# Kernel tuning notes

Hardware: AMD Instinct MI355X
Metric: run time of the kernel (lower is better)

The kernel has to match this reference:

```python
import jax, jax.numpy as jnp
import numpy as np

NUM_VOXELS = 2_000_000
NUM_CLUSTS = 2000
NUM_EDGES = 16_000
IN_FEATS = 4      # columns 1:5 of data: x, y, z, value
HIDDEN = 128
LATENT = 64       # encoder output feature size


def setup_inputs() -> dict:
    key = jax.random.key(0)
    k1, k2, k3, k4, k5, k6, k7 = jax.random.split(key, 7)
    data = jax.random.normal(k1, (NUM_VOXELS, 5), dtype=jnp.float32)
    clust_ids = jax.random.randint(k2, (NUM_VOXELS,), 0, NUM_CLUSTS)
    edge_index = jax.random.randint(k3, (2, NUM_EDGES), 0, NUM_CLUSTS)
    # encoder (pool + MLP) parameters
    W1 = jax.random.normal(k4, (IN_FEATS, HIDDEN), dtype=jnp.float32) / np.sqrt(IN_FEATS)
    b1 = jnp.zeros((HIDDEN,), dtype=jnp.float32)
    W2 = jax.random.normal(k5, (HIDDEN, LATENT), dtype=jnp.float32) / np.sqrt(HIDDEN)
    b2 = jnp.zeros((LATENT,), dtype=jnp.float32)
    return {"data": data, "clust_ids": clust_ids, "edge_index": edge_index,
            "W1": W1, "b1": b1, "W2": W2, "b2": b2}


def reference(data, clust_ids, edge_index, W1, b1, W2, b2):
    # Vectorized replacement of the per-edge python loop:
    # the loop builds, per edge i, the union of voxels of clusters (e0, e1)
    # with batch column overwritten by i; the encoder then globally pools
    # per edge-id. Equivalent: per-cluster sums via one segment_sum pass,
    # then per-edge mean over the union of the two clusters.
    feat = data[:, 1:5]                                   # [N, 4]
    clust_sum = jax.ops.segment_sum(feat, clust_ids, num_segments=NUM_CLUSTS)  # [C, 4]
    clust_cnt = jax.ops.segment_sum(jnp.ones((data.shape[0],), dtype=feat.dtype),
                                    clust_ids, num_segments=NUM_CLUSTS)        # [C]
    e0, e1 = edge_index[0], edge_index[1]
    pooled = (clust_sum[e0] + clust_sum[e1]) / jnp.maximum(clust_cnt[e0] + clust_cnt[e1], 1.0)[:, None]  # [E, 4]
    h = jax.nn.relu(pooled @ W1 + b1)                     # [E, HIDDEN]
    feats = h @ W2 + b2                                   # [E, LATENT]
    return feats
```

## Files before the change

### kernel.cpp

```cpp
#include <hip/hip_runtime.h>

#define NUM_VOXELS 2000000
#define NUM_CLUSTS 2000
#define NUM_EDGES  16000

#define ST   2048
#define ACCN (5 * ST)

#define FSCALE 131072.0f
#define FINV   (1.0f / 131072.0f)

#define A_THREADS 1024
#define A_BLOCKS  512
#define NSLICE (ACCN / 256)
#define RED_CH 64

__device__ __forceinline__ int fxp(float v) {
    return __float2int_rn(v * FSCALE);
}

__global__ __launch_bounds__(A_THREADS) void seg_accum(
        const float* __restrict__ data,
        const int* __restrict__ cids,
        int* __restrict__ part) {
    __shared__ int ls[ACCN];
    for (int o = threadIdx.x; o < ACCN; o += A_THREADS) ls[o] = 0;
    __syncthreads();

    const int ngroups = NUM_VOXELS / 4;
    for (int g = blockIdx.x * A_THREADS + threadIdx.x; g < ngroups;
         g += gridDim.x * A_THREADS) {
        const float4* dp = (const float4*)(data + 20ull * (unsigned)g);
        float4 q0 = dp[0];
        float4 q1 = dp[1];
        float4 q2 = dp[2];
        float4 q3 = dp[3];
        float4 q4 = dp[4];
        int4 c4 = *(const int4*)(cids + 4ull * (unsigned)g);

        atomicAdd(&ls[0 * ST + c4.x], fxp(q0.y));
        atomicAdd(&ls[1 * ST + c4.x], fxp(q0.z));
        atomicAdd(&ls[2 * ST + c4.x], fxp(q0.w));
        atomicAdd(&ls[3 * ST + c4.x], fxp(q1.x));
        atomicAdd(&ls[4 * ST + c4.x], 1);
        atomicAdd(&ls[0 * ST + c4.y], fxp(q1.z));
        atomicAdd(&ls[1 * ST + c4.y], fxp(q1.w));
        atomicAdd(&ls[2 * ST + c4.y], fxp(q2.x));
        atomicAdd(&ls[3 * ST + c4.y], fxp(q2.y));
        atomicAdd(&ls[4 * ST + c4.y], 1);
        atomicAdd(&ls[0 * ST + c4.z], fxp(q2.w));
        atomicAdd(&ls[1 * ST + c4.z], fxp(q3.x));
        atomicAdd(&ls[2 * ST + c4.z], fxp(q3.y));
        atomicAdd(&ls[3 * ST + c4.z], fxp(q3.z));
        atomicAdd(&ls[4 * ST + c4.z], 1);
        atomicAdd(&ls[0 * ST + c4.w], fxp(q4.x));
        atomicAdd(&ls[1 * ST + c4.w], fxp(q4.y));
        atomicAdd(&ls[2 * ST + c4.w], fxp(q4.z));
        atomicAdd(&ls[3 * ST + c4.w], fxp(q4.w));
        atomicAdd(&ls[4 * ST + c4.w], 1);
    }
    __syncthreads();

    int* p = part + (size_t)blockIdx.x * ACCN;
    for (int o = threadIdx.x; o < ACCN; o += A_THREADS) p[o] = ls[o];
}

__global__ __launch_bounds__(A_THREADS) void seg_accum_atomic(
        const float* __restrict__ data,
        const int* __restrict__ cids,
        int* __restrict__ acc) {
    __shared__ int ls[ACCN];
    for (int o = threadIdx.x; o < ACCN; o += A_THREADS) ls[o] = 0;
    __syncthreads();
    const int ngroups = NUM_VOXELS / 4;
    for (int g = blockIdx.x * A_THREADS + threadIdx.x; g < ngroups;
         g += gridDim.x * A_THREADS) {
        const float4* dp = (const float4*)(data + 20ull * (unsigned)g);
        float4 q0 = dp[0], q1 = dp[1], q2 = dp[2], q3 = dp[3], q4 = dp[4];
        int4 c4 = *(const int4*)(cids + 4ull * (unsigned)g);
        atomicAdd(&ls[0 * ST + c4.x], fxp(q0.y));
        atomicAdd(&ls[1 * ST + c4.x], fxp(q0.z));
        atomicAdd(&ls[2 * ST + c4.x], fxp(q0.w));
        atomicAdd(&ls[3 * ST + c4.x], fxp(q1.x));
        atomicAdd(&ls[4 * ST + c4.x], 1);
        atomicAdd(&ls[0 * ST + c4.y], fxp(q1.z));
        atomicAdd(&ls[1 * ST + c4.y], fxp(q1.w));
        atomicAdd(&ls[2 * ST + c4.y], fxp(q2.x));
        atomicAdd(&ls[3 * ST + c4.y], fxp(q2.y));
        atomicAdd(&ls[4 * ST + c4.y], 1);
        atomicAdd(&ls[0 * ST + c4.z], fxp(q2.w));
        atomicAdd(&ls[1 * ST + c4.z], fxp(q3.x));
        atomicAdd(&ls[2 * ST + c4.z], fxp(q3.y));
        atomicAdd(&ls[3 * ST + c4.z], fxp(q3.z));
        atomicAdd(&ls[4 * ST + c4.z], 1);
        atomicAdd(&ls[0 * ST + c4.w], fxp(q4.x));
        atomicAdd(&ls[1 * ST + c4.w], fxp(q4.y));
        atomicAdd(&ls[2 * ST + c4.w], fxp(q4.z));
        atomicAdd(&ls[3 * ST + c4.w], fxp(q4.w));
        atomicAdd(&ls[4 * ST + c4.w], 1);
    }
    __syncthreads();
    for (int o = threadIdx.x; o < ACCN; o += A_THREADS) {
        int v = ls[o];
        if (v != 0) atomicAdd(&acc[o], v);
    }
}

__global__ __launch_bounds__(256) void seg_reduce(
        const int* __restrict__ part, int* __restrict__ acc) {
    const int i = blockIdx.x * 256 + threadIdx.x;
    const int* p = part + (size_t)blockIdx.y * RED_CH * ACCN + i;
    int s0 = 0, s1 = 0, s2 = 0, s3 = 0;
#pragma unroll
    for (int b = 0; b < RED_CH; b += 4) {
        s0 += p[(size_t)(b + 0) * ACCN];
        s1 += p[(size_t)(b + 1) * ACCN];
        s2 += p[(size_t)(b + 2) * ACCN];
        s3 += p[(size_t)(b + 3) * ACCN];
    }
    atomicAdd(&acc[i], (s0 + s1) + (s2 + s3));
}

#define E_BLOCKS 256
#define E_THREADS 256
#define E_WAVES (E_BLOCKS * (E_THREADS / 64))

__global__ __launch_bounds__(E_THREADS) void edge_mlp(
        const int* __restrict__ acc,
        const int* __restrict__ eidx,
        const float* __restrict__ W1, const float* __restrict__ b1,
        const float* __restrict__ W2, const float* __restrict__ b2,
        float* __restrict__ out) {
    __shared__ float sacc[ACCN];
    __shared__ float hbuf[E_THREADS / 64][128];
    const int lane = threadIdx.x & 63;
    const int w = threadIdx.x >> 6;
    const int wg = blockIdx.x * (E_THREADS / 64) + w;

    float w1a[4], w1b[4];
#pragma unroll
    for (int c = 0; c < 4; ++c) {
        w1a[c] = W1[c * 128 + lane];
        w1b[c] = W1[c * 128 + 64 + lane];
    }
    const float b1a = b1[lane];
    const float b1b = b1[64 + lane];
    const float b2j = b2[lane];
    float w2c[128];
#pragma unroll
    for (int k = 0; k < 128; ++k) w2c[k] = W2[k * 64 + lane];

    for (int o = threadIdx.x; o < ACCN; o += E_THREADS) {
        int v = acc[o];
        sacc[o] = (o < 4 * ST) ? (float)v * FINV : (float)v;
    }
    __syncthreads();

    for (int e = wg; e < NUM_EDGES; e += E_WAVES) {
        const int e0 = eidx[e];
        const int e1 = eidx[NUM_EDGES + e];
        const float cnt = sacc[4 * ST + e0] + sacc[4 * ST + e1];
        const float rden = 1.0f / fmaxf(cnt, 1.0f);
        const float p0 = (sacc[0 * ST + e0] + sacc[0 * ST + e1]) * rden;
        const float p1 = (sacc[1 * ST + e0] + sacc[1 * ST + e1]) * rden;
        const float p2 = (sacc[2 * ST + e0] + sacc[2 * ST + e1]) * rden;
        const float p3 = (sacc[3 * ST + e0] + sacc[3 * ST + e1]) * rden;

        float ha = b1a + p0 * w1a[0] + p1 * w1a[1] + p2 * w1a[2] + p3 * w1a[3];
        float hb = b1b + p0 * w1b[0] + p1 * w1b[1] + p2 * w1b[2] + p3 * w1b[3];
        ha = fmaxf(ha, 0.0f);
        hb = fmaxf(hb, 0.0f);

        hbuf[w][lane] = ha;
        hbuf[w][64 + lane] = hb;

        float o0 = b2j;
#pragma unroll
        for (int k = 0; k < 128; k += 4) {
            float4 h4 = *(const float4*)&hbuf[w][k];
            o0 += h4.x * w2c[k] + h4.y * w2c[k + 1] + h4.z * w2c[k + 2] +
                  h4.w * w2c[k + 3];
        }
        out[(size_t)e * 64 + lane] = o0;
    }
}

extern "C" void kernel_launch(void* const* d_in, const int* in_sizes, int n_in,
                              void* d_out, int out_size, void* d_ws, size_t ws_size,
                              hipStream_t stream) {
    const float* data = (const float*)d_in[0];
    const int* cids   = (const int*)d_in[1];
    const int* eidx   = (const int*)d_in[2];
    const float* W1   = (const float*)d_in[3];
    const float* b1   = (const float*)d_in[4];
    const float* W2   = (const float*)d_in[5];
    const float* b2   = (const float*)d_in[6];
    float* out = (float*)d_out;
    int* ws = (int*)d_ws;

    if (ws_size >= (size_t)(A_BLOCKS + 1) * ACCN * sizeof(int)) {
        int* part = ws;
        int* acc = ws + (size_t)A_BLOCKS * ACCN;
        hipMemsetAsync(acc, 0, ACCN * sizeof(int), stream);
        seg_accum<<<A_BLOCKS, A_THREADS, 0, stream>>>(data, cids, part);
        seg_reduce<<<dim3(NSLICE, A_BLOCKS / RED_CH), 256, 0, stream>>>(part, acc);
        edge_mlp<<<E_BLOCKS, E_THREADS, 0, stream>>>(acc, eidx, W1, b1, W2, b2, out);
    } else {
        int* acc = ws;
        hipMemsetAsync(acc, 0, ACCN * sizeof(int), stream);
        seg_accum_atomic<<<A_BLOCKS, A_THREADS, 0, stream>>>(data, cids, acc);
        edge_mlp<<<E_BLOCKS, E_THREADS, 0, stream>>>(acc, eidx, W1, b1, W2, b2, out);
    }
}
```

Baseline: 127.7 us.

## Pack two biased fixed-point sums per 64-bit LDS atomic and drop memset

The voxel accumulation packs two features into one 64-bit shared-memory atomic. Each feature is biased to a positive fixed-point value at a lower scale so the two halves cannot carry into each other, which cuts LDS atomics per voxel from five to three. The final atomic reduce and the memset are replaced by writing per-chunk partials that edge_mlp sums itself. Block count is halved, data loads use nontemporal hints, edge indices are prefetched, and the W2 dot product is split into four accumulators. In exchange, precision drops and correctness relies on per-cluster biased sums fitting in 32 bits.

```diff
diff --git a/kernel.cpp b/kernel.cpp
--- a/kernel.cpp
+++ b/kernel.cpp
@@ -7,57 +7,60 @@
 #define ST   2048
 #define ACCN (5 * ST)
 
-#define FSCALE 131072.0f
-#define FINV   (1.0f / 131072.0f)
-
+#define FSCALE  65536.0f
+#define FINV    (1.0f / 65536.0f)
+#define BIASF   8.0f
+#define BIAS_FS (8.0f * 65536.0f)
+
+#define A_BLOCKS  256
 #define A_THREADS 1024
-#define A_BLOCKS  512
-#define NSLICE (ACCN / 256)
-#define RED_CH 64
-
-__device__ __forceinline__ int fxp(float v) {
-    return __float2int_rn(v * FSCALE);
+#define RED_CH    64
+#define NCH       (A_BLOCKS / RED_CH)
+
+typedef float  f4v __attribute__((ext_vector_type(4)));
+typedef int    i4v __attribute__((ext_vector_type(4)));
+typedef unsigned long long u64;
+
+__device__ __forceinline__ u64 pack2(float a, float b) {
+    unsigned lo = (unsigned)__float2int_rn(fmaf(a, FSCALE, BIAS_FS));
+    unsigned hi = (unsigned)__float2int_rn(fmaf(b, FSCALE, BIAS_FS));
+    return (u64)lo | ((u64)hi << 32);
 }
 
 __global__ __launch_bounds__(A_THREADS) void seg_accum(
         const float* __restrict__ data,
         const int* __restrict__ cids,
         int* __restrict__ part) {
-    __shared__ int ls[ACCN];
+    __shared__ __align__(16) int ls[ACCN];
+    u64* s01 = (u64*)ls;
+    u64* s23 = (u64*)(ls + 4096);
+    int* scnt = ls + 8192;
     for (int o = threadIdx.x; o < ACCN; o += A_THREADS) ls[o] = 0;
     __syncthreads();
 
     const int ngroups = NUM_VOXELS / 4;
     for (int g = blockIdx.x * A_THREADS + threadIdx.x; g < ngroups;
          g += gridDim.x * A_THREADS) {
-        const float4* dp = (const float4*)(data + 20ull * (unsigned)g);
-        float4 q0 = dp[0];
-        float4 q1 = dp[1];
-        float4 q2 = dp[2];
-        float4 q3 = dp[3];
-        float4 q4 = dp[4];
-        int4 c4 = *(const int4*)(cids + 4ull * (unsigned)g);
-
-        atomicAdd(&ls[0 * ST + c4.x], fxp(q0.y));
-        atomicAdd(&ls[1 * ST + c4.x], fxp(q0.z));
-        atomicAdd(&ls[2 * ST + c4.x], fxp(q0.w));
-        atomicAdd(&ls[3 * ST + c4.x], fxp(q1.x));
-        atomicAdd(&ls[4 * ST + c4.x], 1);
-        atomicAdd(&ls[0 * ST + c4.y], fxp(q1.z));
-        atomicAdd(&ls[1 * ST + c4.y], fxp(q1.w));
-        atomicAdd(&ls[2 * ST + c4.y], fxp(q2.x));
-        atomicAdd(&ls[3 * ST + c4.y], fxp(q2.y));
-        atomicAdd(&ls[4 * ST + c4.y], 1);
-        atomicAdd(&ls[0 * ST + c4.z], fxp(q2.w));
-        atomicAdd(&ls[1 * ST + c4.z], fxp(q3.x));
-        atomicAdd(&ls[2 * ST + c4.z], fxp(q3.y));
-        atomicAdd(&ls[3 * ST + c4.z], fxp(q3.z));
-        atomicAdd(&ls[4 * ST + c4.z], 1);
-        atomicAdd(&ls[0 * ST + c4.w], fxp(q4.x));
-        atomicAdd(&ls[1 * ST + c4.w], fxp(q4.y));
-        atomicAdd(&ls[2 * ST + c4.w], fxp(q4.z));
-        atomicAdd(&ls[3 * ST + c4.w], fxp(q4.w));
-        atomicAdd(&ls[4 * ST + c4.w], 1);
+        const f4v* dp = (const f4v*)(data + 20ull * (unsigned)g);
+        f4v q0 = __builtin_nontemporal_load(dp + 0);
+        f4v q1 = __builtin_nontemporal_load(dp + 1);
+        f4v q2 = __builtin_nontemporal_load(dp + 2);
+        f4v q3 = __builtin_nontemporal_load(dp + 3);
+        f4v q4 = __builtin_nontemporal_load(dp + 4);
+        i4v c4 = __builtin_nontemporal_load((const i4v*)(cids + 4ull * (unsigned)g));
+
+        atomicAdd(&s01[c4.x], pack2(q0.y, q0.z));
+        atomicAdd(&s23[c4.x], pack2(q0.w, q1.x));
+        atomicAdd(&scnt[c4.x], 1);
+        atomicAdd(&s01[c4.y], pack2(q1.z, q1.w));
+        atomicAdd(&s23[c4.y], pack2(q2.x, q2.y));
+        atomicAdd(&scnt[c4.y], 1);
+        atomicAdd(&s01[c4.z], pack2(q2.w, q3.x));
+        atomicAdd(&s23[c4.z], pack2(q3.y, q3.z));
+        atomicAdd(&scnt[c4.z], 1);
+        atomicAdd(&s01[c4.w], pack2(q4.x, q4.y));
+        atomicAdd(&s23[c4.w], pack2(q4.z, q4.w));
+        atomicAdd(&scnt[c4.w], 1);
     }
     __syncthreads();
 
@@ -69,35 +72,30 @@
         const float* __restrict__ data,
         const int* __restrict__ cids,
         int* __restrict__ acc) {
-    __shared__ int ls[ACCN];
+    __shared__ __align__(16) int ls[ACCN];
+    u64* s01 = (u64*)ls;
+    u64* s23 = (u64*)(ls + 4096);
+    int* scnt = ls + 8192;
     for (int o = threadIdx.x; o < ACCN; o += A_THREADS) ls[o] = 0;
     __syncthreads();
     const int ngroups = NUM_VOXELS / 4;
     for (int g = blockIdx.x * A_THREADS + threadIdx.x; g < ngroups;
          g += gridDim.x * A_THREADS) {
-        const float4* dp = (const float4*)(data + 20ull * (unsigned)g);
-        float4 q0 = dp[0], q1 = dp[1], q2 = dp[2], q3 = dp[3], q4 = dp[4];
-        int4 c4 = *(const int4*)(cids + 4ull * (unsigned)g);
-        atomicAdd(&ls[0 * ST + c4.x], fxp(q0.y));
-        atomicAdd(&ls[1 * ST + c4.x], fxp(q0.z));
-        atomicAdd(&ls[2 * ST + c4.x], fxp(q0.w));
-        atomicAdd(&ls[3 * ST + c4.x], fxp(q1.x));
-        atomicAdd(&ls[4 * ST + c4.x], 1);
-        atomicAdd(&ls[0 * ST + c4.y], fxp(q1.z));
-        atomicAdd(&ls[1 * ST + c4.y], fxp(q1.w));
-        atomicAdd(&ls[2 * ST + c4.y], fxp(q2.x));
-        atomicAdd(&ls[3 * ST + c4.y], fxp(q2.y));
-        atomicAdd(&ls[4 * ST + c4.y], 1);
-        atomicAdd(&ls[0 * ST + c4.z], fxp(q2.w));
-        atomicAdd(&ls[1 * ST + c4.z], fxp(q3.x));
-        atomicAdd(&ls[2 * ST + c4.z], fxp(q3.y));
-        atomicAdd(&ls[3 * ST + c4.z], fxp(q3.z));
-        atomicAdd(&ls[4 * ST + c4.z], 1);
-        atomicAdd(&ls[0 * ST + c4.w], fxp(q4.x));
-        atomicAdd(&ls[1 * ST + c4.w], fxp(q4.y));
-        atomicAdd(&ls[2 * ST + c4.w], fxp(q4.z));
-        atomicAdd(&ls[3 * ST + c4.w], fxp(q4.w));
-        atomicAdd(&ls[4 * ST + c4.w], 1);
+        const f4v* dp = (const f4v*)(data + 20ull * (unsigned)g);
+        f4v q0 = dp[0], q1 = dp[1], q2 = dp[2], q3 = dp[3], q4 = dp[4];
+        i4v c4 = *(const i4v*)(cids + 4ull * (unsigned)g);
+        atomicAdd(&s01[c4.x], pack2(q0.y, q0.z));
+        atomicAdd(&s23[c4.x], pack2(q0.w, q1.x));
+        atomicAdd(&scnt[c4.x], 1);
+        atomicAdd(&s01[c4.y], pack2(q1.z, q1.w));
+        atomicAdd(&s23[c4.y], pack2(q2.x, q2.y));
+        atomicAdd(&scnt[c4.y], 1);
+        atomicAdd(&s01[c4.z], pack2(q2.w, q3.x));
+        atomicAdd(&s23[c4.z], pack2(q3.y, q3.z));
+        atomicAdd(&scnt[c4.z], 1);
+        atomicAdd(&s01[c4.w], pack2(q4.x, q4.y));
+        atomicAdd(&s23[c4.w], pack2(q4.z, q4.w));
+        atomicAdd(&scnt[c4.w], 1);
     }
     __syncthreads();
     for (int o = threadIdx.x; o < ACCN; o += A_THREADS) {
@@ -107,7 +105,7 @@
 }
 
 __global__ __launch_bounds__(256) void seg_reduce(
-        const int* __restrict__ part, int* __restrict__ acc) {
+        const int* __restrict__ part, int* __restrict__ part2) {
     const int i = blockIdx.x * 256 + threadIdx.x;
     const int* p = part + (size_t)blockIdx.y * RED_CH * ACCN + i;
     int s0 = 0, s1 = 0, s2 = 0, s3 = 0;
@@ -118,7 +116,7 @@
         s2 += p[(size_t)(b + 2) * ACCN];
         s3 += p[(size_t)(b + 3) * ACCN];
     }
-    atomicAdd(&acc[i], (s0 + s1) + (s2 + s3));
+    part2[(size_t)blockIdx.y * ACCN + i] = (s0 + s1) + (s2 + s3);
 }
 
 #define E_BLOCKS 256
@@ -126,7 +124,7 @@
 #define E_WAVES (E_BLOCKS * (E_THREADS / 64))
 
 __global__ __launch_bounds__(E_THREADS) void edge_mlp(
-        const int* __restrict__ acc,
+        const int* __restrict__ part2,
         const int* __restrict__ eidx,
         const float* __restrict__ W1, const float* __restrict__ b1,
         const float* __restrict__ W2, const float* __restrict__ b2,
@@ -151,20 +149,35 @@
     for (int k = 0; k < 128; ++k) w2c[k] = W2[k * 64 + lane];
 
     for (int o = threadIdx.x; o < ACCN; o += E_THREADS) {
-        int v = acc[o];
-        sacc[o] = (o < 4 * ST) ? (float)v * FINV : (float)v;
-    }
-    __syncthreads();
-
+        int s = part2[o] + part2[ACCN + o] + part2[2 * ACCN + o] +
+                part2[3 * ACCN + o];
+        sacc[o] = (o < 8192) ? (float)s * FINV : (float)s;
+    }
+    __syncthreads();
+
+    int e0 = 0, e1 = 0;
+    if (wg < NUM_EDGES) {
+        e0 = eidx[wg];
+        e1 = eidx[NUM_EDGES + wg];
+    }
     for (int e = wg; e < NUM_EDGES; e += E_WAVES) {
-        const int e0 = eidx[e];
-        const int e1 = eidx[NUM_EDGES + e];
-        const float cnt = sacc[4 * ST + e0] + sacc[4 * ST + e1];
+        const int ne = e + E_WAVES;
+        int n0 = 0, n1 = 0;
+        if (ne < NUM_EDGES) {
+            n0 = eidx[ne];
+            n1 = eidx[NUM_EDGES + ne];
+        }
+        const float cnt = sacc[8192 + e0] + sacc[8192 + e1];
         const float rden = 1.0f / fmaxf(cnt, 1.0f);
-        const float p0 = (sacc[0 * ST + e0] + sacc[0 * ST + e1]) * rden;
-        const float p1 = (sacc[1 * ST + e0] + sacc[1 * ST + e1]) * rden;
-        const float p2 = (sacc[2 * ST + e0] + sacc[2 * ST + e1]) * rden;
-        const float p3 = (sacc[3 * ST + e0] + sacc[3 * ST + e1]) * rden;
+        const float bterm = BIASF * cnt;
+        const float r0 = sacc[2 * e0] + sacc[2 * e1];
+        const float r1 = sacc[2 * e0 + 1] + sacc[2 * e1 + 1];
+        const float r2 = sacc[4096 + 2 * e0] + sacc[4096 + 2 * e1];
+        const float r3 = sacc[4096 + 2 * e0 + 1] + sacc[4096 + 2 * e1 + 1];
+        const float p0 = (r0 - bterm) * rden;
+        const float p1 = (r1 - bterm) * rden;
+        const float p2 = (r2 - bterm) * rden;
+        const float p3 = (r3 - bterm) * rden;
 
         float ha = b1a + p0 * w1a[0] + p1 * w1a[1] + p2 * w1a[2] + p3 * w1a[3];
         float hb = b1b + p0 * w1b[0] + p1 * w1b[1] + p2 * w1b[2] + p3 * w1b[3];
@@ -174,14 +187,22 @@
         hbuf[w][lane] = ha;
         hbuf[w][64 + lane] = hb;
 
-        float o0 = b2j;
-#pragma unroll
-        for (int k = 0; k < 128; k += 4) {
-            float4 h4 = *(const float4*)&hbuf[w][k];
-            o0 += h4.x * w2c[k] + h4.y * w2c[k + 1] + h4.z * w2c[k + 2] +
-                  h4.w * w2c[k + 3];
+        float a0 = b2j, a1 = 0.f, a2 = 0.f, a3 = 0.f;
+#pragma unroll
+        for (int k = 0; k < 128; k += 16) {
+            float4 h4;
+            h4 = *(const float4*)&hbuf[w][k];
+            a0 += h4.x * w2c[k] + h4.y * w2c[k + 1] + h4.z * w2c[k + 2] + h4.w * w2c[k + 3];
+            h4 = *(const float4*)&hbuf[w][k + 4];
+            a1 += h4.x * w2c[k + 4] + h4.y * w2c[k + 5] + h4.z * w2c[k + 6] + h4.w * w2c[k + 7];
+            h4 = *(const float4*)&hbuf[w][k + 8];
+            a2 += h4.x * w2c[k + 8] + h4.y * w2c[k + 9] + h4.z * w2c[k + 10] + h4.w * w2c[k + 11];
+            h4 = *(const float4*)&hbuf[w][k + 12];
+            a3 += h4.x * w2c[k + 12] + h4.y * w2c[k + 13] + h4.z * w2c[k + 14] + h4.w * w2c[k + 15];
         }
-        out[(size_t)e * 64 + lane] = o0;
+        out[(size_t)e * 64 + lane] = (a0 + a1) + (a2 + a3);
+        e0 = n0;
+        e1 = n1;
     }
 }
 
@@ -198,17 +219,16 @@
     float* out = (float*)d_out;
     int* ws = (int*)d_ws;
 
-    if (ws_size >= (size_t)(A_BLOCKS + 1) * ACCN * sizeof(int)) {
-        int* part = ws;
-        int* acc = ws + (size_t)A_BLOCKS * ACCN;
-        hipMemsetAsync(acc, 0, ACCN * sizeof(int), stream);
+    if (ws_size >= (size_t)(A_BLOCKS + NCH) * ACCN * sizeof(int)) {
+        int* part  = ws;
+        int* part2 = ws + (size_t)A_BLOCKS * ACCN;
         seg_accum<<<A_BLOCKS, A_THREADS, 0, stream>>>(data, cids, part);
-        seg_reduce<<<dim3(NSLICE, A_BLOCKS / RED_CH), 256, 0, stream>>>(part, acc);
-        edge_mlp<<<E_BLOCKS, E_THREADS, 0, stream>>>(acc, eidx, W1, b1, W2, b2, out);
+        seg_reduce<<<dim3(ACCN / 256, NCH), 256, 0, stream>>>(part, part2);
+        edge_mlp<<<E_BLOCKS, E_THREADS, 0, stream>>>(part2, eidx, W1, b1, W2, b2, out);
     } else {
-        int* acc = ws;
-        hipMemsetAsync(acc, 0, ACCN * sizeof(int), stream);
-        seg_accum_atomic<<<A_BLOCKS, A_THREADS, 0, stream>>>(data, cids, acc);
-        edge_mlp<<<E_BLOCKS, E_THREADS, 0, stream>>>(acc, eidx, W1, b1, W2, b2, out);
-    }
-}
+        int* part2 = ws;
+        hipMemsetAsync(part2, 0, (size_t)NCH * ACCN * sizeof(int), stream);
+        seg_accum_atomic<<<A_BLOCKS, A_THREADS, 0, stream>>>(data, cids, part2);
+        edge_mlp<<<E_BLOCKS, E_THREADS, 0, stream>>>(part2, eidx, W1, b1, W2, b2, out);
+    }
+}
```

After: 147.1 us. 1.15x slower.
